# Kernel tuning notes

Measured on AMD Instinct MI355X. Metric: run time of the kernel, lower is better.

Reference implementation:

```python
import jax, jax.numpy as jnp
import numpy as np

BASE_RES = 16; DESIRED_RES = 8192; LEVEL_INTERVAL = 2
LEVEL_DIM = 4; LOG2_HASH = 21
NUM_LEVELS = int(np.log(DESIRED_RES / BASE_RES) / np.log(LEVEL_INTERVAL)) + 1  # 10
MAX_PARAMS = 2 ** LOG2_HASH

def _level_metas():
    s = np.exp2(np.log2(DESIRED_RES / BASE_RES) / (NUM_LEVELS - 1))  # per-level scale = 2
    metas, off = [], 0
    for l in range(NUM_LEVELS):
        scale = BASE_RES * s ** l - 1.0
        res = int(np.ceil(scale)) + 1
        dense = res ** 3 <= MAX_PARAMS
        size = res ** 3 if dense else MAX_PARAMS
        size = int(np.ceil(size / 8) * 8)
        metas.append((scale, res, size, off, dense))
        off += size
    return metas, off

METAS, TABLE_SIZE = _level_metas()  # TABLE_SIZE = 14979072
OUT_DIM = NUM_LEVELS * LEVEL_DIM    # 40
PRIMES = (np.uint32(1), np.uint32(2654435761), np.uint32(805459861))

def contract(x):
    n = jnp.sqrt(jnp.maximum(jnp.sum(x * x, -1, keepdims=True), 1e-12))
    return jnp.where(n <= 1.0, x, (2.0 - 1.0 / n) * (x / n))

def grid_encode(x, table):
    # x: [N,3] in [0,1]; table: [TABLE_SIZE, LEVEL_DIM]. Multi-res hash grid, trilinear, align_corners=False.
    feats = []
    for scale, res, size, off, dense in METAS:
        pos = x * scale + 0.5
        p0f = jnp.floor(pos)
        f = pos - p0f  # trilinear fractions [N,3]
        p0 = p0f.astype(jnp.uint32)
        lvl = table[off:off + size]
        out = jnp.zeros((x.shape[0], LEVEL_DIM), x.dtype)
        for dx in (0, 1):
            for dy in (0, 1):
                for dz in (0, 1):
                    cx = p0[:, 0] + np.uint32(dx)
                    cy = p0[:, 1] + np.uint32(dy)
                    cz = p0[:, 2] + np.uint32(dz)
                    w = ((f[:, 0] if dx else 1.0 - f[:, 0]) *
                         (f[:, 1] if dy else 1.0 - f[:, 1]) *
                         (f[:, 2] if dz else 1.0 - f[:, 2]))
                    if dense:
                        idx = (cx * np.uint32(res) + cy) * np.uint32(res) + cz
                    else:
                        idx = (cx * PRIMES[0]) ^ (cy * PRIMES[1]) ^ (cz * PRIMES[2])
                    idx = (idx % np.uint32(size)).astype(jnp.int32)
                    out = out + w[:, None] * lvl[idx]
        feats.append(out)
    return jnp.concatenate(feats, -1)

def dir_enc(d):
    # pos_enc min_deg=0, max_deg=4, with_identity -> 3 + 2*3*4 = 27 dims
    scales = (2.0 ** jnp.arange(4)).astype(d.dtype)
    xb = (d[..., None, :] * scales[:, None]).reshape(d.shape[:-1] + (12,))
    return jnp.concatenate([d, jnp.sin(jnp.concatenate([xb, xb + 0.5 * jnp.pi], -1))], -1)

def _forward(coords, viewdirs, table, Wd0, bd0, Wd1, bd1, W0, b0, W1, b1, Wr, br):
    c = contract(coords) / 2.0          # warp_fn='contract', bound=2
    x01 = (c + 1.0) * 0.5               # encoder normalizes [-1,1] -> [0,1]
    N = int(np.prod(coords.shape[:-1]))
    feats = grid_encode(x01.reshape(N, 3), table).reshape(coords.shape[:-1] + (OUT_DIM,))
    h = jax.nn.relu(feats @ Wd0 + bd0)
    x = h @ Wd1 + bd1                   # bottleneck [..., 256]
    density = jax.nn.softplus(x[..., 0] - 1.0)  # density_bias = -1
    de = dir_enc(viewdirs)
    de = jnp.broadcast_to(de[..., None, :], x.shape[:-1] + (de.shape[-1],))
    inp = jnp.concatenate([x, de], -1)  # [..., 283]
    h = jax.nn.relu(inp @ W0 + b0)
    h = jnp.concatenate([h, inp], -1)   # skip at layer 0 -> [..., 539]
    h = jax.nn.relu(h @ W1 + b1)
    rgb = jax.nn.sigmoid(h @ Wr + br)   # premultiplier=1, rgb_bias=0
    rgb = rgb * (1.0 + 2 * 0.001) - 0.001  # rgb_padding
    return jnp.concatenate([density[..., None], rgb], -1)  # [..., 4]


def setup_inputs() -> dict:
    key = jax.random.key(0)
    ks = jax.random.split(key, 8)
    B, S = 4096, 32
    coords = jax.random.normal(ks[0], (B, S, 3), jnp.float32) * 1.5
    vd = jax.random.normal(ks[1], (B, 3), jnp.float32)
    viewdirs = vd / jnp.linalg.norm(vd, axis=-1, keepdims=True)
    table = jax.random.uniform(ks[2], (TABLE_SIZE, LEVEL_DIM), jnp.float32, -1e-4, 1e-4)
    def lin(k, i, o):
        s = 1.0 / np.sqrt(i)
        return jax.random.uniform(k, (i, o), jnp.float32, -s, s)
    BW, DE, NW = 256, 27, 256
    return dict(coords=coords, viewdirs=viewdirs, table=table,
                Wd0=lin(ks[3], OUT_DIM, 64), bd0=jnp.zeros((64,), jnp.float32),
                Wd1=lin(ks[4], 64, BW), bd1=jnp.zeros((BW,), jnp.float32),
                W0=lin(ks[5], BW + DE, NW), b0=jnp.zeros((NW,), jnp.float32),
                W1=lin(ks[6], NW + BW + DE, NW), b1=jnp.zeros((NW,), jnp.float32),
                Wr=lin(ks[7], NW, 3), br=jnp.zeros((3,), jnp.float32))


def reference(coords, viewdirs, table, Wd0, bd0, Wd1, bd1, W0, b0, W1, b1, Wr, br):
    return _forward(coords, viewdirs, table, Wd0, bd0, Wd1, bd1, W0, b0, W1, b1, Wr, br)
```

## Files before the change

### kernel.cpp

```cpp
#include <hip/hip_runtime.h>
#include <hip/hip_bf16.h>

#define NPTS (4096 * 32)

typedef __bf16 bf16x8 __attribute__((ext_vector_type(8)));
typedef float f32x4 __attribute__((ext_vector_type(4)));

__device__ __forceinline__ float bf2f(unsigned short u) {
    union { unsigned u32; float f; } v;
    v.u32 = ((unsigned)u) << 16;
    return v.f;
}
__device__ __forceinline__ unsigned short f2bf(float f) {
    __hip_bfloat16 h = __float2bfloat16(f);
    union { __hip_bfloat16 h; unsigned short u; } v;
    v.h = h;
    return v.u;
}

static __device__ const float    LVL_SCALE[10] = {15.f,31.f,63.f,127.f,255.f,511.f,1023.f,2047.f,4095.f,8191.f};
static __device__ const unsigned LVL_RES[10]   = {16u,32u,64u,128u,256u,512u,1024u,2048u,4096u,8192u};
static __device__ const unsigned LVL_OFF[10]   = {0u,4096u,36864u,299008u,2396160u,4493312u,6590464u,8687616u,10784768u,12881920u};
static __device__ const unsigned LVL_MASK[10]  = {4095u,32767u,262143u,2097151u,2097151u,2097151u,2097151u,2097151u,2097151u};

__global__ __launch_bounds__(256) void k_encode(const float* __restrict__ coords,
                                                const float* __restrict__ table,
                                                unsigned short* __restrict__ featsb) {
    int n = blockIdx.x * 256 + threadIdx.x;
    float x = coords[(size_t)n*3+0], y = coords[(size_t)n*3+1], z = coords[(size_t)n*3+2];
    float sq = x*x + y*y + z*z;
    float nn = sqrtf(fmaxf(sq, 1e-12f));
    if (nn > 1.0f) {
        float inv = 1.0f / nn;
        float s = 2.0f - inv;
        x = s * (x * inv); y = s * (y * inv); z = s * (z * inv);
    }
    float px = (x * 0.5f + 1.0f) * 0.5f;
    float py = (y * 0.5f + 1.0f) * 0.5f;
    float pz = (z * 0.5f + 1.0f) * 0.5f;
    const float4* tab = (const float4*)table;
    unsigned short* fr = featsb + (size_t)n * 64;
#pragma unroll
    for (int l = 0; l < 10; ++l) {
        float sc = LVL_SCALE[l];
        unsigned res = LVL_RES[l], mask = LVL_MASK[l];
        const float4* tl = tab + LVL_OFF[l];
        float fx = px*sc + 0.5f, fy = py*sc + 0.5f, fz = pz*sc + 0.5f;
        float x0 = floorf(fx), y0 = floorf(fy), z0 = floorf(fz);
        float tx = fx - x0, ty = fy - y0, tz = fz - z0;
        unsigned cx = (unsigned)x0, cy = (unsigned)y0, cz = (unsigned)z0;
        float ax = 0.f, ay = 0.f, az = 0.f, aw = 0.f;
#pragma unroll
        for (int dx = 0; dx < 2; ++dx)
#pragma unroll
        for (int dy = 0; dy < 2; ++dy)
#pragma unroll
        for (int dz = 0; dz < 2; ++dz) {
            unsigned ux = cx + dx, uy = cy + dy, uz = cz + dz;
            unsigned idx;
            if (l < 4) idx = ((ux * res + uy) * res + uz) & mask;
            else       idx = (ux ^ (uy * 2654435761u) ^ (uz * 805459861u)) & mask;
            float w = (dx ? tx : 1.0f - tx) * (dy ? ty : 1.0f - ty) * (dz ? tz : 1.0f - tz);
            float4 v = tl[idx];
            ax += w * v.x; ay += w * v.y; az += w * v.z; aw += w * v.w;
        }
        ushort4 s;
        s.x = f2bf(ax); s.y = f2bf(ay); s.z = f2bf(az); s.w = f2bf(aw);
        *(ushort4*)(fr + l * 4) = s;
    }
    ushort4 z4; z4.x = z4.y = z4.z = z4.w = 0;
#pragma unroll
    for (int k = 40; k < 64; k += 4) *(ushort4*)(fr + k) = z4;
}

__global__ __launch_bounds__(256) void k_prep(const float* __restrict__ W0,
                                              const float* __restrict__ W1,
                                              const float* __restrict__ Wd0,
                                              const float* __restrict__ Wd1,
                                              unsigned short* __restrict__ W0t,
                                              unsigned short* __restrict__ W1t,
                                              unsigned short* __restrict__ Wd0t,
                                              unsigned short* __restrict__ Wd1t) {
    int i = blockIdx.x * 256 + threadIdx.x;
    if (i < 65536) {
        int c = i >> 8, k = i & 255;
        W0t[i] = f2bf(W0[(size_t)k * 256 + c]);
    }
    {
        int c = i >> 9, k = i & 511;
        W1t[i] = f2bf(W1[(size_t)k * 256 + c]);
    }
    if (i < 4608) {
        int c = i / 72, k = i % 72;
        Wd0t[i] = (k < 40) ? f2bf(Wd0[(size_t)k * 64 + c]) : 0;
    }
    if (i < 18432) {
        int c = i / 72, k = i % 72;
        Wd1t[i] = (k < 64) ? f2bf(Wd1[(size_t)k * 256 + c]) : 0;
    }
}

__global__ __launch_bounds__(256) void k_dirw(const float* __restrict__ vd,
                                              const float* __restrict__ W0,
                                              const float* __restrict__ b0,
                                              const float* __restrict__ W1,
                                              const float* __restrict__ b1,
                                              float* __restrict__ deW0,
                                              float* __restrict__ deW1) {
    __shared__ float de[27];
    int b = blockIdx.x;
    int t = threadIdx.x;
    if (t < 27) {
        float v;
        const float HPI = 0.5f * 3.14159265358979323846f;
        if (t < 3) {
            v = vd[(size_t)b*3 + t];
        } else if (t < 15) {
            int i = (t - 3) / 3, j = (t - 3) % 3;
            v = sinf(vd[(size_t)b*3 + j] * (float)(1 << i));
        } else {
            int i = (t - 15) / 3, j = (t - 15) % 3;
            v = sinf(vd[(size_t)b*3 + j] * (float)(1 << i) + HPI);
        }
        de[t] = v;
    }
    __syncthreads();
    float a0 = b0[t], a1 = b1[t];
#pragma unroll
    for (int k = 0; k < 27; ++k) {
        float d = de[k];
        a0 += d * W0[(size_t)(256 + k) * 256 + t];
        a1 += d * W1[(size_t)(512 + k) * 256 + t];
    }
    deW0[(size_t)b*256 + t] = a0;
    deW1[(size_t)b*256 + t] = a1;
}

__global__ __launch_bounds__(512, 4) void k_mlp0(const unsigned short* __restrict__ featsb,
                                                 const unsigned short* __restrict__ Wd0t,
                                                 const unsigned short* __restrict__ Wd1t,
                                                 const float* __restrict__ bd0,
                                                 const float* __restrict__ bd1,
                                                 unsigned short* __restrict__ xb,
                                                 float* __restrict__ out) {
    __shared__ __align__(16) unsigned short sWd1[256 * 72];
    __shared__ __align__(16) unsigned short sWd0[64 * 72];
    __shared__ __align__(16) unsigned short sF[64 * 72];
    __shared__ __align__(16) unsigned short sH[64 * 72];
    int t = threadIdx.x;
    int r0 = blockIdx.x * 64;
    {
        int r = t >> 3, kq = (t & 7) * 8;
        *(int4*)(sF + r * 72 + kq)   = *(const int4*)(featsb + (size_t)(r0 + r) * 64 + kq);
        *(int4*)(sWd0 + r * 72 + kq) = *(const int4*)(Wd0t + r * 72 + kq);
#pragma unroll
        for (int j = 0; j < 4; ++j) {
            int idx = t + j * 512;
            int c = idx >> 3, k = (idx & 7) * 8;
            *(int4*)(sWd1 + c * 72 + k) = *(const int4*)(Wd1t + c * 72 + k);
        }
    }
    __syncthreads();
    int lane = t & 63, wid = t >> 6, cl = lane & 15, q = lane >> 4;
    {
        int wr = wid >> 1, wc = wid & 1;
        f32x4 acc[2] = {};
#pragma unroll
        for (int ks = 0; ks < 2; ++ks) {
            bf16x8 af = *(const bf16x8*)(sF + (wr * 16 + cl) * 72 + ks * 32 + q * 8);
#pragma unroll
            for (int n = 0; n < 2; ++n) {
                bf16x8 bf = *(const bf16x8*)(sWd0 + (wc * 32 + n * 16 + cl) * 72 + ks * 32 + q * 8);
                acc[n] = __builtin_amdgcn_mfma_f32_16x16x32_bf16(af, bf, acc[n], 0, 0, 0);
            }
        }
#pragma unroll
        for (int n = 0; n < 2; ++n) {
            int c = wc * 32 + n * 16 + cl;
            float bv = bd0[c];
#pragma unroll
            for (int i = 0; i < 4; ++i) {
                int r = wr * 16 + q * 4 + i;
                sH[r * 72 + c] = f2bf(fmaxf(acc[n][i] + bv, 0.f));
            }
        }
    }
    __syncthreads();
    {
        int wr = wid >> 2, wc = wid & 3;
        f32x4 acc[2][4] = {};
#pragma unroll
        for (int ks = 0; ks < 2; ++ks) {
            bf16x8 af[2], bf[4];
#pragma unroll
            for (int m = 0; m < 2; ++m)
                af[m] = *(const bf16x8*)(sH + (wr * 32 + m * 16 + cl) * 72 + ks * 32 + q * 8);
#pragma unroll
            for (int n = 0; n < 4; ++n)
                bf[n] = *(const bf16x8*)(sWd1 + (wc * 64 + n * 16 + cl) * 72 + ks * 32 + q * 8);
#pragma unroll
            for (int m = 0; m < 2; ++m)
#pragma unroll
                for (int n = 0; n < 4; ++n)
                    acc[m][n] = __builtin_amdgcn_mfma_f32_16x16x32_bf16(af[m], bf[n], acc[m][n], 0, 0, 0);
        }
#pragma unroll
        for (int n = 0; n < 4; ++n) {
            int c = wc * 64 + n * 16 + cl;
            float bv = bd1[c];
#pragma unroll
            for (int m = 0; m < 2; ++m) {
#pragma unroll
                for (int i = 0; i < 4; ++i) {
                    int r = wr * 32 + m * 16 + q * 4 + i;
                    float v = acc[m][n][i] + bv;
                    xb[(size_t)(r0 + r) * 256 + c] = f2bf(v);
                    if (n == 0 && wc == 0 && cl == 0) {
                        float d = v - 1.0f;
                        float sp = fmaxf(d, 0.0f) + log1pf(expf(-fabsf(d)));
                        out[(size_t)(r0 + r) * 4] = sp;
                    }
                }
            }
        }
    }
}

template<int KT, bool G4>
__global__ __launch_bounds__(512, 4) void k_gemm(const unsigned short* __restrict__ A0,
                                                 const unsigned short* __restrict__ A1,
                                                 const unsigned short* __restrict__ Bt,
                                                 const float* __restrict__ dw,
                                                 const float* __restrict__ Wr,
                                                 const float* __restrict__ br,
                                                 unsigned short* __restrict__ Ho,
                                                 float* __restrict__ out) {
    __shared__ __align__(16) unsigned short smem[23040];
    __shared__ float sWr[256 * 3];
    unsigned short* sA = smem;
    unsigned short* sB = smem + 64 * 72;
    int t = threadIdx.x;
    int lane = t & 63, wid = t >> 6;
    int wr = wid >> 2, wc = wid & 3;
    int cl = lane & 15, q = lane >> 4;
    int r0 = blockIdx.x * 64;

    if constexpr (G4) {
        for (int i = t; i < 768; i += 512) sWr[i] = Wr[i];
    }

    f32x4 acc[2][4] = {};

    int ar = t >> 3, ak = (t & 7) * 8;
    int bc = t >> 1, bk = (t & 1) * 32;
    const unsigned short* Bp0 = Bt + (size_t)bc * KT + bk;

    for (int k0 = 0; k0 < KT; k0 += 64) {
        const unsigned short* As;
        int ka;
        if constexpr (G4) { As = (k0 >= 256) ? A1 : A0; ka = k0 & 255; }
        else              { As = A0; ka = k0; }
        int4 av  = *(const int4*)(As + (size_t)(r0 + ar) * 256 + ka + ak);
        int4 bv0 = *(const int4*)(Bp0 + k0);
        int4 bv1 = *(const int4*)(Bp0 + k0 + 8);
        int4 bv2 = *(const int4*)(Bp0 + k0 + 16);
        int4 bv3 = *(const int4*)(Bp0 + k0 + 24);
        __syncthreads();
        *(int4*)(sA + ar * 72 + ak)      = av;
        *(int4*)(sB + bc * 72 + bk)      = bv0;
        *(int4*)(sB + bc * 72 + bk + 8)  = bv1;
        *(int4*)(sB + bc * 72 + bk + 16) = bv2;
        *(int4*)(sB + bc * 72 + bk + 24) = bv3;
        __syncthreads();
#pragma unroll
        for (int kk = 0; kk < 2; ++kk) {
            int ko = kk * 32 + q * 8;
            bf16x8 af[2], bf[4];
#pragma unroll
            for (int m = 0; m < 2; ++m)
                af[m] = *(const bf16x8*)(sA + (wr * 32 + m * 16 + cl) * 72 + ko);
#pragma unroll
            for (int n = 0; n < 4; ++n)
                bf[n] = *(const bf16x8*)(sB + (wc * 64 + n * 16 + cl) * 72 + ko);
#pragma unroll
            for (int m = 0; m < 2; ++m)
#pragma unroll
                for (int n = 0; n < 4; ++n)
                    acc[m][n] = __builtin_amdgcn_mfma_f32_16x16x32_bf16(af[m], bf[n], acc[m][n], 0, 0, 0);
        }
    }

    __syncthreads();

    if constexpr (!G4) {
#pragma unroll
        for (int m = 0; m < 2; ++m) {
            int rb = wr * 32 + m * 16;
            const float* dwp = dw + (size_t)((r0 + rb) >> 5) * 256;
#pragma unroll
            for (int n = 0; n < 4; ++n) {
                int c = wc * 64 + n * 16 + cl;
                float dv = dwp[c];
#pragma unroll
                for (int i = 0; i < 4; ++i) {
                    int r = rb + q * 4 + i;
                    Ho[(size_t)(r0 + r) * 256 + c] = f2bf(fmaxf(acc[m][n][i] + dv, 0.f));
                }
            }
        }
    } else {
        unsigned short* sH = smem;
#pragma unroll
        for (int m = 0; m < 2; ++m) {
            int rb = wr * 32 + m * 16;
            const float* dwp = dw + (size_t)((r0 + rb) >> 5) * 256;
#pragma unroll
            for (int n = 0; n < 4; ++n) {
                int c = wc * 64 + n * 16 + cl;
                float dv = dwp[c];
#pragma unroll
                for (int i = 0; i < 4; ++i) {
                    int r = rb + q * 4 + i;
                    sH[r * 264 + c] = f2bf(fmaxf(acc[m][n][i] + dv, 0.f));
                }
            }
        }
        __syncthreads();
        if (t < 384) {
            int r = t / 6, rem = t % 6, j = rem >> 1, half = rem & 1;
            float a = 0.f;
            const unsigned short* hp = sH + r * 264 + half * 128;
            const float* wp = sWr + (half * 128) * 3 + j;
            for (int c = 0; c < 128; ++c) a += bf2f(hp[c]) * wp[c * 3];
            a += __shfl_xor(a, 1);
            if (!half) {
                a += br[j];
                float s = 1.0f / (1.0f + expf(-a));
                out[(size_t)(r0 + r) * 4 + 1 + j] = s * 1.002f - 0.001f;
            }
        }
    }
}

extern "C" void kernel_launch(void* const* d_in, const int* in_sizes, int n_in,
                              void* d_out, int out_size, void* d_ws, size_t ws_size,
                              hipStream_t stream) {
    const float* coords   = (const float*)d_in[0];
    const float* viewdirs = (const float*)d_in[1];
    const float* table    = (const float*)d_in[2];
    const float* Wd0      = (const float*)d_in[3];
    const float* bd0      = (const float*)d_in[4];
    const float* Wd1      = (const float*)d_in[5];
    const float* bd1      = (const float*)d_in[6];
    const float* W0       = (const float*)d_in[7];
    const float* b0       = (const float*)d_in[8];
    const float* W1       = (const float*)d_in[9];
    const float* b1       = (const float*)d_in[10];
    const float* Wr       = (const float*)d_in[11];
    const float* br       = (const float*)d_in[12];
    float* out = (float*)d_out;

    const size_t N = NPTS;
    unsigned short* ws = (unsigned short*)d_ws;
    unsigned short* featsb = ws;
    unsigned short* xb     = featsb + N * 64;
    unsigned short* h0b    = xb + N * 256;
    float* deW0 = (float*)(h0b + N * 256);
    float* deW1 = deW0 + 4096 * 256;
    unsigned short* W0t  = (unsigned short*)(deW1 + 4096 * 256);
    unsigned short* W1t  = W0t + 65536;
    unsigned short* Wd0t = W1t + 131072;
    unsigned short* Wd1t = Wd0t + 4608;

    k_encode<<<NPTS / 256, 256, 0, stream>>>(coords, table, featsb);
    k_prep<<<512, 256, 0, stream>>>(W0, W1, Wd0, Wd1, W0t, W1t, Wd0t, Wd1t);
    k_dirw<<<4096, 256, 0, stream>>>(viewdirs, W0, b0, W1, b1, deW0, deW1);
    k_mlp0<<<NPTS / 64, 512, 0, stream>>>(featsb, Wd0t, Wd1t, bd0, bd1, xb, out);
    k_gemm<256, false><<<NPTS / 64, 512, 0, stream>>>(xb, nullptr, W0t,
                                                      deW0, nullptr, nullptr,
                                                      h0b, nullptr);
    k_gemm<512, true><<<NPTS / 64, 512, 0, stream>>>(h0b, xb, W1t,
                                                     deW1, Wr, br, nullptr, out);
}
```

Baseline: 270.6 us.

## Fuse the two MLP GEMMs into one kernel and split encoding across thread pairs

Merges the layer-0 and layer-1 GEMMs into a single kernel. The intermediate h0 activation stays in shared memory instead of round-tripping through global memory, and the xb A-operand is loaded once for both its GEMM contributions. This removes the h0b write and read plus one launch, in exchange for lower occupancy (launch bounds 512,2) and more LDS per block. The hash-grid encoder now uses two threads per point, each handling five interleaved levels, to expose more parallelism for the latency-bound gathers. The cost is recomputing the contraction per thread and adding per-thread selects for the level parameters.

```diff
diff --git a/kernel.cpp b/kernel.cpp
--- a/kernel.cpp
+++ b/kernel.cpp
@@ -18,15 +18,11 @@
     return v.u;
 }
 
-static __device__ const float    LVL_SCALE[10] = {15.f,31.f,63.f,127.f,255.f,511.f,1023.f,2047.f,4095.f,8191.f};
-static __device__ const unsigned LVL_RES[10]   = {16u,32u,64u,128u,256u,512u,1024u,2048u,4096u,8192u};
-static __device__ const unsigned LVL_OFF[10]   = {0u,4096u,36864u,299008u,2396160u,4493312u,6590464u,8687616u,10784768u,12881920u};
-static __device__ const unsigned LVL_MASK[10]  = {4095u,32767u,262143u,2097151u,2097151u,2097151u,2097151u,2097151u,2097151u};
-
 __global__ __launch_bounds__(256) void k_encode(const float* __restrict__ coords,
                                                 const float* __restrict__ table,
                                                 unsigned short* __restrict__ featsb) {
-    int n = blockIdx.x * 256 + threadIdx.x;
+    int id = blockIdx.x * 256 + threadIdx.x;
+    int n = id >> 1, p = id & 1;
     float x = coords[(size_t)n*3+0], y = coords[(size_t)n*3+1], z = coords[(size_t)n*3+2];
     float sq = x*x + y*y + z*z;
     float nn = sqrtf(fmaxf(sq, 1e-12f));
@@ -40,11 +36,18 @@
     float pz = (z * 0.5f + 1.0f) * 0.5f;
     const float4* tab = (const float4*)table;
     unsigned short* fr = featsb + (size_t)n * 64;
-#pragma unroll
-    for (int l = 0; l < 10; ++l) {
-        float sc = LVL_SCALE[l];
-        unsigned res = LVL_RES[l], mask = LVL_MASK[l];
-        const float4* tl = tab + LVL_OFF[l];
+    constexpr unsigned OFFS[10] = {0u,4096u,36864u,299008u,2396160u,4493312u,6590464u,8687616u,10784768u,12881920u};
+#pragma unroll
+    for (int j = 0; j < 5; ++j) {
+        int l2 = 2 * j;
+        unsigned res   = p ? (16u << (l2+1)) : (16u << l2);
+        float sc       = (float)(res - 1u);
+        unsigned mask  = (l2+1 < 4 || !p) && (l2 < 4)
+                         ? ((p ? (1u << (12+3*(l2+1))) : (1u << (12+3*l2))) - 1u)
+                         : 2097151u;
+        unsigned off   = p ? OFFS[l2+1] : OFFS[l2];
+        bool dense     = (p ? (l2+1) : l2) < 4;
+        const float4* tl = tab + off;
         float fx = px*sc + 0.5f, fy = py*sc + 0.5f, fz = pz*sc + 0.5f;
         float x0 = floorf(fx), y0 = floorf(fy), z0 = floorf(fz);
         float tx = fx - x0, ty = fy - y0, tz = fz - z0;
@@ -58,7 +61,7 @@
         for (int dz = 0; dz < 2; ++dz) {
             unsigned ux = cx + dx, uy = cy + dy, uz = cz + dz;
             unsigned idx;
-            if (l < 4) idx = ((ux * res + uy) * res + uz) & mask;
+            if (dense) idx = ((ux * res + uy) * res + uz) & mask;
             else       idx = (ux ^ (uy * 2654435761u) ^ (uz * 805459861u)) & mask;
             float w = (dx ? tx : 1.0f - tx) * (dy ? ty : 1.0f - ty) * (dz ? tz : 1.0f - tz);
             float4 v = tl[idx];
@@ -66,11 +69,11 @@
         }
         ushort4 s;
         s.x = f2bf(ax); s.y = f2bf(ay); s.z = f2bf(az); s.w = f2bf(aw);
-        *(ushort4*)(fr + l * 4) = s;
+        *(ushort4*)(fr + (l2 + p) * 4) = s;
     }
     ushort4 z4; z4.x = z4.y = z4.z = z4.w = 0;
 #pragma unroll
-    for (int k = 40; k < 64; k += 4) *(ushort4*)(fr + k) = z4;
+    for (int k = 40 + p * 4; k < 64; k += 8) *(ushort4*)(fr + k) = z4;
 }
 
 __global__ __launch_bounds__(256) void k_prep(const float* __restrict__ W0,
@@ -226,118 +229,140 @@
     }
 }
 
-template<int KT, bool G4>
-__global__ __launch_bounds__(512, 4) void k_gemm(const unsigned short* __restrict__ A0,
-                                                 const unsigned short* __restrict__ A1,
-                                                 const unsigned short* __restrict__ Bt,
-                                                 const float* __restrict__ dw,
-                                                 const float* __restrict__ Wr,
-                                                 const float* __restrict__ br,
-                                                 unsigned short* __restrict__ Ho,
-                                                 float* __restrict__ out) {
-    __shared__ __align__(16) unsigned short smem[23040];
-    __shared__ float sWr[256 * 3];
-    unsigned short* sA = smem;
-    unsigned short* sB = smem + 64 * 72;
+__global__ __launch_bounds__(512, 2) void k_g34(const unsigned short* __restrict__ xb,
+                                                const unsigned short* __restrict__ W0t,
+                                                const unsigned short* __restrict__ W1t,
+                                                const float* __restrict__ deW0,
+                                                const float* __restrict__ deW1,
+                                                const float* __restrict__ Wr,
+                                                const float* __restrict__ br,
+                                                float* __restrict__ out) {
+    __shared__ __align__(16) unsigned short sH0[4][64 * 72];
+    __shared__ __align__(16) unsigned short sB[256 * 40];
+    __shared__ float sWr[768];
     int t = threadIdx.x;
     int lane = t & 63, wid = t >> 6;
     int wr = wid >> 2, wc = wid & 3;
     int cl = lane & 15, q = lane >> 4;
     int r0 = blockIdx.x * 64;
-
-    if constexpr (G4) {
-        for (int i = t; i < 768; i += 512) sWr[i] = Wr[i];
-    }
-
-    f32x4 acc[2][4] = {};
-
-    int ar = t >> 3, ak = (t & 7) * 8;
-    int bc = t >> 1, bk = (t & 1) * 32;
-    const unsigned short* Bp0 = Bt + (size_t)bc * KT + bk;
-
-    for (int k0 = 0; k0 < KT; k0 += 64) {
-        const unsigned short* As;
-        int ka;
-        if constexpr (G4) { As = (k0 >= 256) ? A1 : A0; ka = k0 & 255; }
-        else              { As = A0; ka = k0; }
-        int4 av  = *(const int4*)(As + (size_t)(r0 + ar) * 256 + ka + ak);
-        int4 bv0 = *(const int4*)(Bp0 + k0);
-        int4 bv1 = *(const int4*)(Bp0 + k0 + 8);
-        int4 bv2 = *(const int4*)(Bp0 + k0 + 16);
-        int4 bv3 = *(const int4*)(Bp0 + k0 + 24);
-        __syncthreads();
-        *(int4*)(sA + ar * 72 + ak)      = av;
-        *(int4*)(sB + bc * 72 + bk)      = bv0;
-        *(int4*)(sB + bc * 72 + bk + 8)  = bv1;
-        *(int4*)(sB + bc * 72 + bk + 16) = bv2;
-        *(int4*)(sB + bc * 72 + bk + 24) = bv3;
-        __syncthreads();
-#pragma unroll
-        for (int kk = 0; kk < 2; ++kk) {
-            int ko = kk * 32 + q * 8;
-            bf16x8 af[2], bf[4];
+    for (int i = t; i < 768; i += 512) sWr[i] = Wr[i];
+
+    int bc = t >> 1, bh = (t & 1) * 16;
+    const unsigned short* W0p = W0t + (size_t)bc * 256 + bh;
+    const unsigned short* W1p = W1t + (size_t)bc * 512 + bh;
+    const unsigned short* Arow0 = xb + (size_t)(r0 + wr * 32 + cl) * 256 + q * 8;
+    const unsigned short* Arow1 = Arow0 + 16 * 256;
+
+    f32x4 acc1[2][4] = {};
+    f32x4 acc2[2][4] = {};
+
+    for (int c8 = 0; c8 < 8; ++c8) {
+        int k0 = c8 * 32;
+        bf16x8 af[2];
+        af[0] = *(const bf16x8*)(Arow0 + k0);
+        af[1] = *(const bf16x8*)(Arow1 + k0);
+        int4 b0 = *(const int4*)(W0p + k0);
+        int4 b1 = *(const int4*)(W0p + k0 + 8);
+        __syncthreads();
+        *(int4*)(sB + bc * 40 + bh)     = b0;
+        *(int4*)(sB + bc * 40 + bh + 8) = b1;
+        __syncthreads();
+        {
+            bf16x8 bf[4];
+#pragma unroll
+            for (int n = 0; n < 4; ++n)
+                bf[n] = *(const bf16x8*)(sB + (wc * 64 + n * 16 + cl) * 40 + q * 8);
 #pragma unroll
             for (int m = 0; m < 2; ++m)
-                af[m] = *(const bf16x8*)(sA + (wr * 32 + m * 16 + cl) * 72 + ko);
+#pragma unroll
+                for (int n = 0; n < 4; ++n)
+                    acc1[m][n] = __builtin_amdgcn_mfma_f32_16x16x32_bf16(af[m], bf[n], acc1[m][n], 0, 0, 0);
+        }
+        int4 c0 = *(const int4*)(W1p + 256 + k0);
+        int4 c1 = *(const int4*)(W1p + 256 + k0 + 8);
+        __syncthreads();
+        *(int4*)(sB + bc * 40 + bh)     = c0;
+        *(int4*)(sB + bc * 40 + bh + 8) = c1;
+        __syncthreads();
+        {
+            bf16x8 bf[4];
 #pragma unroll
             for (int n = 0; n < 4; ++n)
-                bf[n] = *(const bf16x8*)(sB + (wc * 64 + n * 16 + cl) * 72 + ko);
+                bf[n] = *(const bf16x8*)(sB + (wc * 64 + n * 16 + cl) * 40 + q * 8);
 #pragma unroll
             for (int m = 0; m < 2; ++m)
 #pragma unroll
                 for (int n = 0; n < 4; ++n)
-                    acc[m][n] = __builtin_amdgcn_mfma_f32_16x16x32_bf16(af[m], bf[n], acc[m][n], 0, 0, 0);
-        }
-    }
-
-    __syncthreads();
-
-    if constexpr (!G4) {
-#pragma unroll
-        for (int m = 0; m < 2; ++m) {
-            int rb = wr * 32 + m * 16;
-            const float* dwp = dw + (size_t)((r0 + rb) >> 5) * 256;
-#pragma unroll
-            for (int n = 0; n < 4; ++n) {
-                int c = wc * 64 + n * 16 + cl;
-                float dv = dwp[c];
-#pragma unroll
-                for (int i = 0; i < 4; ++i) {
-                    int r = rb + q * 4 + i;
-                    Ho[(size_t)(r0 + r) * 256 + c] = f2bf(fmaxf(acc[m][n][i] + dv, 0.f));
-                }
+                    acc2[m][n] = __builtin_amdgcn_mfma_f32_16x16x32_bf16(af[m], bf[n], acc2[m][n], 0, 0, 0);
+        }
+    }
+#pragma unroll
+    for (int m = 0; m < 2; ++m) {
+        int rb = wr * 32 + m * 16;
+        const float* dwp = deW0 + (size_t)((r0 + rb) >> 5) * 256;
+#pragma unroll
+        for (int n = 0; n < 4; ++n) {
+            int c = wc * 64 + n * 16 + cl;
+            float dv = dwp[c];
+#pragma unroll
+            for (int i = 0; i < 4; ++i) {
+                int r = rb + q * 4 + i;
+                sH0[wc][r * 72 + (c & 63)] = f2bf(fmaxf(acc1[m][n][i] + dv, 0.f));
             }
         }
-    } else {
-        unsigned short* sH = smem;
-#pragma unroll
-        for (int m = 0; m < 2; ++m) {
-            int rb = wr * 32 + m * 16;
-            const float* dwp = dw + (size_t)((r0 + rb) >> 5) * 256;
-#pragma unroll
-            for (int n = 0; n < 4; ++n) {
-                int c = wc * 64 + n * 16 + cl;
-                float dv = dwp[c];
-#pragma unroll
-                for (int i = 0; i < 4; ++i) {
-                    int r = rb + q * 4 + i;
-                    sH[r * 264 + c] = f2bf(fmaxf(acc[m][n][i] + dv, 0.f));
-                }
+    }
+    __syncthreads();
+    for (int c8 = 0; c8 < 8; ++c8) {
+        int k0 = c8 * 32;
+        bf16x8 af[2];
+#pragma unroll
+        for (int m = 0; m < 2; ++m)
+            af[m] = *(const bf16x8*)(&sH0[k0 >> 6][(wr * 32 + m * 16 + cl) * 72 + (k0 & 63) + q * 8]);
+        int4 b0 = *(const int4*)(W1p + k0);
+        int4 b1 = *(const int4*)(W1p + k0 + 8);
+        __syncthreads();
+        *(int4*)(sB + bc * 40 + bh)     = b0;
+        *(int4*)(sB + bc * 40 + bh + 8) = b1;
+        __syncthreads();
+        bf16x8 bf[4];
+#pragma unroll
+        for (int n = 0; n < 4; ++n)
+            bf[n] = *(const bf16x8*)(sB + (wc * 64 + n * 16 + cl) * 40 + q * 8);
+#pragma unroll
+        for (int m = 0; m < 2; ++m)
+#pragma unroll
+            for (int n = 0; n < 4; ++n)
+                acc2[m][n] = __builtin_amdgcn_mfma_f32_16x16x32_bf16(af[m], bf[n], acc2[m][n], 0, 0, 0);
+    }
+    __syncthreads();
+    unsigned short* sH1 = &sH0[0][0];
+#pragma unroll
+    for (int m = 0; m < 2; ++m) {
+        int rb = wr * 32 + m * 16;
+        const float* dwp = deW1 + (size_t)((r0 + rb) >> 5) * 256;
+#pragma unroll
+        for (int n = 0; n < 4; ++n) {
+            int c = wc * 64 + n * 16 + cl;
+            float dv = dwp[c];
+#pragma unroll
+            for (int i = 0; i < 4; ++i) {
+                int r = rb + q * 4 + i;
+                sH1[r * 264 + c] = f2bf(fmaxf(acc2[m][n][i] + dv, 0.f));
             }
         }
-        __syncthreads();
-        if (t < 384) {
-            int r = t / 6, rem = t % 6, j = rem >> 1, half = rem & 1;
-            float a = 0.f;
-            const unsigned short* hp = sH + r * 264 + half * 128;
-            const float* wp = sWr + (half * 128) * 3 + j;
-            for (int c = 0; c < 128; ++c) a += bf2f(hp[c]) * wp[c * 3];
-            a += __shfl_xor(a, 1);
-            if (!half) {
-                a += br[j];
-                float s = 1.0f / (1.0f + expf(-a));
-                out[(size_t)(r0 + r) * 4 + 1 + j] = s * 1.002f - 0.001f;
-            }
+    }
+    __syncthreads();
+    if (t < 384) {
+        int r = t / 6, rem = t % 6, j = rem >> 1, half = rem & 1;
+        float a = 0.f;
+        const unsigned short* hp = sH1 + r * 264 + half * 128;
+        const float* wp = sWr + (half * 128) * 3 + j;
+        for (int c = 0; c < 128; ++c) a += bf2f(hp[c]) * wp[c * 3];
+        a += __shfl_xor(a, 1);
+        if (!half) {
+            a += br[j];
+            float s = 1.0f / (1.0f + expf(-a));
+            out[(size_t)(r0 + r) * 4 + 1 + j] = s * 1.002f - 0.001f;
         }
     }
 }
@@ -364,21 +389,16 @@
     unsigned short* ws = (unsigned short*)d_ws;
     unsigned short* featsb = ws;
     unsigned short* xb     = featsb + N * 64;
-    unsigned short* h0b    = xb + N * 256;
-    float* deW0 = (float*)(h0b + N * 256);
+    float* deW0 = (float*)(xb + N * 256);
     float* deW1 = deW0 + 4096 * 256;
     unsigned short* W0t  = (unsigned short*)(deW1 + 4096 * 256);
     unsigned short* W1t  = W0t + 65536;
     unsigned short* Wd0t = W1t + 131072;
     unsigned short* Wd1t = Wd0t + 4608;
 
-    k_encode<<<NPTS / 256, 256, 0, stream>>>(coords, table, featsb);
+    k_encode<<<NPTS / 128, 256, 0, stream>>>(coords, table, featsb);
     k_prep<<<512, 256, 0, stream>>>(W0, W1, Wd0, Wd1, W0t, W1t, Wd0t, Wd1t);
     k_dirw<<<4096, 256, 0, stream>>>(viewdirs, W0, b0, W1, b1, deW0, deW1);
     k_mlp0<<<NPTS / 64, 512, 0, stream>>>(featsb, Wd0t, Wd1t, bd0, bd1, xb, out);
-    k_gemm<256, false><<<NPTS / 64, 512, 0, stream>>>(xb, nullptr, W0t,
-                                                      deW0, nullptr, nullptr,
-                                                      h0b, nullptr);
-    k_gemm<512, true><<<NPTS / 64, 512, 0, stream>>>(h0b, xb, W1t,
-                                                     deW1, Wr, br, nullptr, out);
-}
+    k_g34<<<NPTS / 64, 512, 0, stream>>>(xb, W0t, W1t, deW0, deW1, Wr, br, out);
+}
```

Result: slower. 278.6 us (+2.9%).
